# Optimization experiments

Hardware: AMD Instinct MI355X
Metric: run time of the kernel (lower is better)

## Reference

```python
import jax, jax.numpy as jnp
import numpy as np

IN_FEATURES = 4096
OUT_FEATURES = 4096
ALPHA = 0.008

def setup_inputs() -> dict:
    key = jax.random.key(0)
    k_x, k_w = jax.random.split(key)
    # int8-valued activations and weights, stored as their natural int/float forms
    x = jax.random.randint(k_x, (4, 2048, IN_FEATURES), -127, 128, dtype=jnp.int32)
    weight = jax.random.randint(k_w, (OUT_FEATURES, IN_FEATURES), -127, 128, dtype=jnp.int32).astype(jnp.float32)
    bias = jnp.zeros((1, OUT_FEATURES), dtype=jnp.float32)  # fp16 in module; fp32 here for math
    alpha = jnp.float32(ALPHA)
    return {"x": x, "weight": weight, "bias": bias, "alpha": alpha}

def reference(x, weight, bias, alpha):
    # x: [B, S, in], weight: [out, in] (int8 values cast to fp32), bias: [1, out]
    # In the original, rand_elements/mask_mul are zeros so hybrid path == plain path:
    #   y = F.linear(x.float(), weight.float()); fp_y = y*alpha + bias
    x_shape = x.shape
    xf = x.reshape(-1, x_shape[-1]).astype(jnp.float32)  # [N, in]
    y = jnp.einsum('ni,oi->no', xf, weight)              # fp32 GEMM, as in the module
    fp_y = y * alpha + bias
    out = jnp.clip(jnp.round(fp_y), -128, 127).astype(jnp.int8)
    return out.reshape(*x_shape[:-1], -1)
```

## Files before the change

kernel.cpp:

```cpp
#include <hip/hip_runtime.h>
#include <stdint.h>

typedef int int32x4  __attribute__((ext_vector_type(4)));
typedef int int32x16 __attribute__((ext_vector_type(16)));

#define IN_F   4096
#define OUT_F  4096
#define ROWS   8192

#define BM 128
#define BN 128
#define BK 128

#define GLOAD_LDS16(g, l)                                                      \
  __builtin_amdgcn_global_load_lds(                                            \
      (const __attribute__((address_space(1))) void*)(g),                      \
      (__attribute__((address_space(3))) void*)(l), 16, 0, 0)

__device__ __forceinline__ int pack4i(int a, int b, int c, int d) {
  return (a & 0xff) | ((b & 0xff) << 8) | ((c & 0xff) << 16) | (d << 24);
}

#define XB 32768
#define WB 16384
__global__ void __launch_bounds__(256) cvt_kernel(const int4* __restrict__ x,
                                                  const float4* __restrict__ w,
                                                  int* __restrict__ ox,
                                                  int* __restrict__ ow) {
  int b = blockIdx.x;
  if (b < XB) {
    size_t i = (size_t)b * 256 + threadIdx.x;
    int4 a = x[i];
    ox[i] = pack4i(a.x, a.y, a.z, a.w);
  } else {
    size_t i = (size_t)(b - XB) * 256 + threadIdx.x;
    float4 a = w[i];
    ow[i] = pack4i(__float2int_rn(a.x), __float2int_rn(a.y),
                   __float2int_rn(a.z), __float2int_rn(a.w));
  }
}

__global__ void __launch_bounds__(256) gemm_i8_kernel(
    const int8_t* __restrict__ A8, const int8_t* __restrict__ B8,
    const float* __restrict__ bias, const float* __restrict__ alpha_p,
    int* __restrict__ out) {
  __shared__ int8_t As[BM * BK];
  __shared__ int8_t Bs[BN * BK];

  const int t = threadIdx.x;
  const int wave = t >> 6;
  const int lane = t & 63;
  const int l31 = lane & 31;
  const int hi  = lane >> 5;
  const int wm = wave >> 1;
  const int wn = wave & 1;

  const int bn = blockIdx.x;
  const int bm = blockIdx.y;

  const int rowS = t >> 3;
  const int colS = ((t & 7) ^ (rowS & 7)) * 16;
  const int8_t* ag = A8 + (size_t)(bm * BM + rowS) * IN_F + colS;
  const int8_t* bg = B8 + (size_t)(bn * BN + rowS) * IN_F + colS;
  int8_t* la = As + t * 16;
  int8_t* lb = Bs + t * 16;

  const int32x4* As4 = (const int32x4*)As;
  const int32x4* Bs4 = (const int32x4*)Bs;
  const int swz = l31 & 7;
  const int arow0 = (wm * 64 + l31) * 8;
  const int brow0 = (wn * 64 + l31) * 8;

  int32x16 acc[2][2] = {};

  for (int k0 = 0; k0 < IN_F; k0 += BK) {
#pragma unroll
    for (int j = 0; j < 4; ++j) {
      GLOAD_LDS16(ag + k0 + (size_t)(32 * j) * IN_F, la + 4096 * j);
      GLOAD_LDS16(bg + k0 + (size_t)(32 * j) * IN_F, lb + 4096 * j);
    }
    __syncthreads();

#pragma unroll
    for (int ks = 0; ks < 4; ++ks) {
      const int ksw = (ks * 2 + hi) ^ swz;
      int32x4 af[2], bf[2];
#pragma unroll
      for (int i = 0; i < 2; ++i) af[i] = As4[arow0 + i * 256 + ksw];
#pragma unroll
      for (int i = 0; i < 2; ++i) bf[i] = Bs4[brow0 + i * 256 + ksw];
#pragma unroll
      for (int mi = 0; mi < 2; ++mi)
#pragma unroll
        for (int ni = 0; ni < 2; ++ni)
          acc[mi][ni] = __builtin_amdgcn_mfma_i32_32x32x32_i8(
              af[mi], bf[ni], acc[mi][ni], 0, 0, 0);
    }
    __syncthreads();
  }

  const float alpha = *alpha_p;
#pragma unroll
  for (int mi = 0; mi < 2; ++mi) {
    const int rowt = bm * BM + wm * 64 + mi * 32 + hi * 4;
#pragma unroll
    for (int ni = 0; ni < 2; ++ni) {
      const int col = bn * BN + wn * 64 + ni * 32 + l31;
      const float bv = bias[col];
#pragma unroll
      for (int r = 0; r < 16; ++r) {
        const int row = rowt + (r & 3) + 8 * (r >> 2);
        float v = rintf((float)acc[mi][ni][r] * alpha + bv);
        v = fminf(fmaxf(v, -128.f), 127.f);
        out[(size_t)row * OUT_F + col] = (int)v;
      }
    }
  }
}

extern "C" void kernel_launch(void* const* d_in, const int* in_sizes, int n_in,
                              void* d_out, int out_size, void* d_ws, size_t ws_size,
                              hipStream_t stream) {
  const int*   x     = (const int*)d_in[0];
  const float* w     = (const float*)d_in[1];
  const float* bias  = (const float*)d_in[2];
  const float* alpha = (const float*)d_in[3];
  int* out = (int*)d_out;

  int8_t* x8 = (int8_t*)d_ws;
  int8_t* w8 = x8 + (size_t)ROWS * IN_F;

  cvt_kernel<<<XB + WB, 256, 0, stream>>>((const int4*)x, (const float4*)w,
                                          (int*)x8, (int*)w8);

  dim3 grid(OUT_F / BN, ROWS / BM);
  gemm_i8_kernel<<<grid, 256, 0, stream>>>(x8, w8, bias, alpha, out);
}
```

Before: 402.7 us.

## Use 256x256 tiles with 4-stage async LDS pipeline and grid-stride convert

Enlarges the GEMM block tile to 256x256 with 512 threads and BK=64, using a 4-buffer LDS ring (128KB dynamic) so global-to-LDS loads for three tiles ahead overlap MFMA compute, with one barrier per tile instead of two. It adds a block-index swizzle for L2 locality, raises wave priority around MFMA bursts, and turns the convert kernel into a grid-stride loop over fewer blocks. The large LDS footprint limits occupancy to one block per CU, and the grid drops to 512 blocks, which risks poorer load balance across CUs.

```diff
diff --git a/kernel.cpp b/kernel.cpp
--- a/kernel.cpp
+++ b/kernel.cpp
@@ -8,101 +8,137 @@
 #define OUT_F  4096
 #define ROWS   8192
 
-#define BM 128
-#define BN 128
-#define BK 128
+#define BM 256
+#define BN 256
+#define BK 64
+#define NT (IN_F / BK)
+#define TILE_LDS 32768
+#define LDS_TOTAL (4 * TILE_LDS)
 
 #define GLOAD_LDS16(g, l)                                                      \
   __builtin_amdgcn_global_load_lds(                                            \
       (const __attribute__((address_space(1))) void*)(g),                      \
       (__attribute__((address_space(3))) void*)(l), 16, 0, 0)
 
+#define WAITV(n)                                                               \
+  do {                                                                         \
+    asm volatile("s_waitcnt vmcnt(" #n ")" ::: "memory");                      \
+    __builtin_amdgcn_sched_barrier(0);                                         \
+  } while (0)
+
 __device__ __forceinline__ int pack4i(int a, int b, int c, int d) {
   return (a & 0xff) | ((b & 0xff) << 8) | ((c & 0xff) << 16) | (d << 24);
 }
 
-#define XB 32768
-#define WB 16384
+#define CVT_BLOCKS 2048
+#define CVT_NX 8388608
+#define CVT_NT 12582912
 __global__ void __launch_bounds__(256) cvt_kernel(const int4* __restrict__ x,
                                                   const float4* __restrict__ w,
                                                   int* __restrict__ ox,
                                                   int* __restrict__ ow) {
-  int b = blockIdx.x;
-  if (b < XB) {
-    size_t i = (size_t)b * 256 + threadIdx.x;
-    int4 a = x[i];
-    ox[i] = pack4i(a.x, a.y, a.z, a.w);
-  } else {
-    size_t i = (size_t)(b - XB) * 256 + threadIdx.x;
-    float4 a = w[i];
-    ow[i] = pack4i(__float2int_rn(a.x), __float2int_rn(a.y),
-                   __float2int_rn(a.z), __float2int_rn(a.w));
+  size_t i = (size_t)blockIdx.x * 256 + threadIdx.x;
+  for (; i < CVT_NT; i += (size_t)CVT_BLOCKS * 256) {
+    if (i < CVT_NX) {
+      int4 a = x[i];
+      ox[i] = pack4i(a.x, a.y, a.z, a.w);
+    } else {
+      size_t j = i - CVT_NX;
+      float4 a = w[j];
+      ow[j] = pack4i(__float2int_rn(a.x), __float2int_rn(a.y),
+                     __float2int_rn(a.z), __float2int_rn(a.w));
+    }
   }
 }
 
-__global__ void __launch_bounds__(256) gemm_i8_kernel(
+__global__ void __launch_bounds__(512) gemm_i8_kernel(
     const int8_t* __restrict__ A8, const int8_t* __restrict__ B8,
     const float* __restrict__ bias, const float* __restrict__ alpha_p,
     int* __restrict__ out) {
-  __shared__ int8_t As[BM * BK];
-  __shared__ int8_t Bs[BN * BK];
+  extern __shared__ int8_t lds[];
 
-  const int t = threadIdx.x;
+  const int t    = threadIdx.x;
   const int wave = t >> 6;
   const int lane = t & 63;
-  const int l31 = lane & 31;
-  const int hi  = lane >> 5;
-  const int wm = wave >> 1;
-  const int wn = wave & 1;
+  const int l31  = lane & 31;
+  const int hi   = lane >> 5;
+  const int wm   = wave >> 2;
+  const int wn   = wave & 3;
 
-  const int bn = blockIdx.x;
-  const int bm = blockIdx.y;
+  const int flat = blockIdx.y * gridDim.x + blockIdx.x;
+  const int wid  = (flat & 7) * 64 + (flat >> 3);
+  const int bm   = wid >> 4;
+  const int bn   = wid & 15;
 
-  const int rowS = t >> 3;
-  const int colS = ((t & 7) ^ (rowS & 7)) * 16;
-  const int8_t* ag = A8 + (size_t)(bm * BM + rowS) * IN_F + colS;
-  const int8_t* bg = B8 + (size_t)(bn * BN + rowS) * IN_F + colS;
-  int8_t* la = As + t * 16;
-  int8_t* lb = Bs + t * 16;
+  const int rS = t >> 2;
+  const int cS = ((t & 3) ^ ((t >> 3) & 3)) * 16;
+  const int8_t* ga = A8 + (size_t)(bm * BM + rS) * IN_F + cS;
+  const int8_t* gb = B8 + (size_t)(bn * BN + rS) * IN_F + cS;
+  const int ldst = t * 16;
 
-  const int32x4* As4 = (const int32x4*)As;
-  const int32x4* Bs4 = (const int32x4*)Bs;
-  const int swz = l31 & 7;
-  const int arow0 = (wm * 64 + l31) * 8;
-  const int brow0 = (wn * 64 + l31) * 8;
+  const int swz   = (l31 >> 1) & 3;
+  const int arow0 = (wm * 128 + l31) * 4;
+  const int brow0 = (wn * 64  + l31) * 4;
 
-  int32x16 acc[2][2] = {};
+  int32x16 acc[4][2] = {};
 
-  for (int k0 = 0; k0 < IN_F; k0 += BK) {
+  auto issue = [&](int tile) {
+    int8_t* base = lds + (tile & 3) * TILE_LDS;
+    const int k0 = tile * BK;
+    GLOAD_LDS16(ga + k0,                      base + ldst);
+    GLOAD_LDS16(ga + k0 + (size_t)128 * IN_F, base + 8192  + ldst);
+    GLOAD_LDS16(gb + k0,                      base + 16384 + ldst);
+    GLOAD_LDS16(gb + k0 + (size_t)128 * IN_F, base + 24576 + ldst);
+  };
+
+  auto compute = [&](int tile) {
+    const int32x4* As4 = (const int32x4*)(lds + (tile & 3) * TILE_LDS);
+    const int32x4* Bs4 = (const int32x4*)(lds + (tile & 3) * TILE_LDS + 16384);
 #pragma unroll
-    for (int j = 0; j < 4; ++j) {
-      GLOAD_LDS16(ag + k0 + (size_t)(32 * j) * IN_F, la + 4096 * j);
-      GLOAD_LDS16(bg + k0 + (size_t)(32 * j) * IN_F, lb + 4096 * j);
-    }
-    __syncthreads();
-
+    for (int ks = 0; ks < 2; ++ks) {
+      const int ksw = (ks * 2 + hi) ^ swz;
+      int32x4 af[4], bf[2];
 #pragma unroll
-    for (int ks = 0; ks < 4; ++ks) {
-      const int ksw = (ks * 2 + hi) ^ swz;
-      int32x4 af[2], bf[2];
+      for (int i = 0; i < 4; ++i) af[i] = As4[arow0 + i * 128 + ksw];
 #pragma unroll
-      for (int i = 0; i < 2; ++i) af[i] = As4[arow0 + i * 256 + ksw];
+      for (int i = 0; i < 2; ++i) bf[i] = Bs4[brow0 + i * 128 + ksw];
+      __builtin_amdgcn_s_setprio(1);
 #pragma unroll
-      for (int i = 0; i < 2; ++i) bf[i] = Bs4[brow0 + i * 256 + ksw];
-#pragma unroll
-      for (int mi = 0; mi < 2; ++mi)
+      for (int mi = 0; mi < 4; ++mi)
 #pragma unroll
         for (int ni = 0; ni < 2; ++ni)
           acc[mi][ni] = __builtin_amdgcn_mfma_i32_32x32x32_i8(
               af[mi], bf[ni], acc[mi][ni], 0, 0, 0);
+      __builtin_amdgcn_s_setprio(0);
     }
-    __syncthreads();
+  };
+
+  issue(0); issue(1); issue(2);
+
+  for (int tt = 0; tt < NT - 3; ++tt) {
+    WAITV(8);
+    __builtin_amdgcn_s_barrier();
+    __builtin_amdgcn_sched_barrier(0);
+    issue(tt + 3);
+    compute(tt);
   }
+  WAITV(8);
+  __builtin_amdgcn_s_barrier();
+  __builtin_amdgcn_sched_barrier(0);
+  compute(NT - 3);
+  WAITV(4);
+  __builtin_amdgcn_s_barrier();
+  __builtin_amdgcn_sched_barrier(0);
+  compute(NT - 2);
+  WAITV(0);
+  __builtin_amdgcn_s_barrier();
+  __builtin_amdgcn_sched_barrier(0);
+  compute(NT - 1);
 
   const float alpha = *alpha_p;
 #pragma unroll
-  for (int mi = 0; mi < 2; ++mi) {
-    const int rowt = bm * BM + wm * 64 + mi * 32 + hi * 4;
+  for (int mi = 0; mi < 4; ++mi) {
+    const int rowt = bm * BM + wm * 128 + mi * 32 + hi * 4;
 #pragma unroll
     for (int ni = 0; ni < 2; ++ni) {
       const int col = bn * BN + wn * 64 + ni * 32 + l31;
@@ -130,9 +166,17 @@
   int8_t* x8 = (int8_t*)d_ws;
   int8_t* w8 = x8 + (size_t)ROWS * IN_F;
 
-  cvt_kernel<<<XB + WB, 256, 0, stream>>>((const int4*)x, (const float4*)w,
-                                          (int*)x8, (int*)w8);
+  static bool attr_done = false;
+  if (!attr_done) {
+    (void)hipFuncSetAttribute(reinterpret_cast<const void*>(gemm_i8_kernel),
+                              hipFuncAttributeMaxDynamicSharedMemorySize,
+                              LDS_TOTAL);
+    attr_done = true;
+  }
+
+  cvt_kernel<<<CVT_BLOCKS, 256, 0, stream>>>((const int4*)x, (const float4*)w,
+                                             (int*)x8, (int*)w8);
 
   dim3 grid(OUT_F / BN, ROWS / BM);
-  gemm_i8_kernel<<<grid, 256, 0, stream>>>(x8, w8, bias, alpha, out);
+  gemm_i8_kernel<<<grid, 512, LDS_TOTAL, stream>>>(x8, w8, bias, alpha, out);
 }
```

Measured after the change: 407.4 us. Within noise of the previous version (+1.2%).
